# Kernel tuning notes

Hardware: AMD Instinct MI355X
Metric: run time of the kernel (lower is better)

Reference implementation:

```python
import jax, jax.numpy as jnp
import numpy as np

# Model dims (MiniCPM-style decode-only LM inside VoxCPM2)
L, B, D = 16, 4, 1024
H, HD, KVH = 16, 64, 8          # query heads, head dim, KV heads (GQA)
DFF = 4096
S = 2048                         # current KV cache length
SCALE_DEPTH = 1.4                # mup depth scaling
EPS = 1e-5
THETA = 10000.0
W_STD = 0.02


def setup_inputs() -> dict:
    key = jax.random.key(0)
    ks = jax.random.split(key, 12)
    return {
        "inputs_embeds": jax.random.normal(ks[0], (B, D), jnp.float32),
        "k_cache": jax.random.normal(ks[1], (L, B, KVH, S, HD), jnp.float32),
        "v_cache": jax.random.normal(ks[2], (L, B, KVH, S, HD), jnp.float32),
        "ln1_w": jnp.ones((L, D), jnp.float32),
        "ln2_w": jnp.ones((L, D), jnp.float32),
        "norm_w": jnp.ones((D,), jnp.float32),
        "wq": jax.random.normal(ks[3], (L, D, H * HD), jnp.float32) * W_STD,
        "wk": jax.random.normal(ks[4], (L, D, KVH * HD), jnp.float32) * W_STD,
        "wv": jax.random.normal(ks[5], (L, D, KVH * HD), jnp.float32) * W_STD,
        "wo": jax.random.normal(ks[6], (L, H * HD, D), jnp.float32) * W_STD,
        "w_gate": jax.random.normal(ks[7], (L, D, DFF), jnp.float32) * W_STD,
        "w_up": jax.random.normal(ks[8], (L, D, DFF), jnp.float32) * W_STD,
        "w_down": jax.random.normal(ks[9], (L, DFF, D), jnp.float32) * W_STD,
        "cache_length": S,  # position id of the token being decoded
    }


def _rmsnorm(x, w):
    return x * jax.lax.rsqrt(jnp.mean(x * x, axis=-1, keepdims=True) + EPS) * w


def _rotate_half(x):
    x1, x2 = jnp.split(x, 2, axis=-1)
    return jnp.concatenate((-x2, x1), axis=-1)


def _decode_step(inputs_embeds, k_cache, v_cache, ln1_w, ln2_w, norm_w,
                 wq, wk, wv, wo, w_gate, w_up, w_down, cache_length):
    # RoPE tables for the single decode position
    pos = jnp.asarray(cache_length, jnp.float32)
    inv_freq = 1.0 / (THETA ** (jnp.arange(0, HD, 2, dtype=jnp.float32) / HD))
    freqs = pos * inv_freq                       # [HD/2]
    emb = jnp.concatenate((freqs, freqs))        # [HD]
    cos, sin = jnp.cos(emb), jnp.sin(emb)

    mup = SCALE_DEPTH / np.sqrt(L)
    scale = 1.0 / np.sqrt(HD)
    G = H // KVH  # query heads per KV head

    def layer(h, ws):
        l1, l2, Wq, Wk, Wv, Wo, Wg, Wu, Wd, kc, vc = ws
        x = _rmsnorm(h, l1)                                  # [B, D]
        q = (x @ Wq).reshape(B, H, HD)
        k = (x @ Wk).reshape(B, KVH, HD)
        v = (x @ Wv).reshape(B, KVH, HD)
        q = q * cos + _rotate_half(q) * sin
        k = k * cos + _rotate_half(k) * sin
        nk = jnp.concatenate((kc, k[:, :, None, :]), axis=2)  # [B, KVH, S+1, HD]
        nv = jnp.concatenate((vc, v[:, :, None, :]), axis=2)
        qg = q.reshape(B, KVH, G, HD)                         # GQA grouping
        scores = jnp.einsum('bkgd,bksd->bkgs', qg, nk) * scale
        p = jax.nn.softmax(scores, axis=-1)
        o = jnp.einsum('bkgs,bksd->bkgd', p, nv).reshape(B, H * HD)
        h = h + (o @ Wo) * mup                                # mup residual
        x = _rmsnorm(h, l2)
        mlp = (jax.nn.silu(x @ Wg) * (x @ Wu)) @ Wd           # SwiGLU
        h = h + mlp * mup
        return h, (nk, nv)

    h, (next_k, next_v) = jax.lax.scan(
        layer, inputs_embeds,
        (ln1_w, ln2_w, wq, wk, wv, wo, w_gate, w_up, w_down, k_cache, v_cache))
    h = _rmsnorm(h, norm_w)
    return h, next_k, next_v


def reference(inputs_embeds, k_cache, v_cache, ln1_w, ln2_w, norm_w,
              wq, wk, wv, wo, w_gate, w_up, w_down, cache_length):
    h, nk, nv = _decode_step(inputs_embeds, k_cache, v_cache, ln1_w, ln2_w,
                             norm_w, wq, wk, wv, wo, w_gate, w_up, w_down,
                             cache_length)
    return h, nk, nv, jnp.asarray(cache_length + 1, jnp.int64)
```

## Files before the change

### kernel.cpp

```cpp
#include <hip/hip_runtime.h>
#include <math.h>

#define MUP 0.35f
#define SCALE 0.125f
#define EPS 1e-5f

#define WS_HA    0
#define WS_HB    4096
#define WS_YMLP  8192
#define WS_YO    12288
#define WS_QKVP  16384
#define WS_GUP   16384
#define WS_OPART 278528

#define OUT_NK  4096
#define OUT_NV  (4096 + 16*4*8*2049*64)
#define OUT_SC  (4096 + 2*16*4*8*2049*64)

__device__ __forceinline__ float wsum64(float v) {
    v += __shfl_xor(v, 32); v += __shfl_xor(v, 16); v += __shfl_xor(v, 8);
    v += __shfl_xor(v, 4);  v += __shfl_xor(v, 2);  v += __shfl_xor(v, 1);
    return v;
}

__device__ __forceinline__ void fma4(float4& a, float s, const float4 w) {
    a.x = fmaf(s, w.x, a.x); a.y = fmaf(s, w.y, a.y);
    a.z = fmaf(s, w.z, a.z); a.w = fmaf(s, w.w, a.w);
}

__global__ __launch_bounds__(256) void k_init(const float* __restrict__ emb,
                                              const int* __restrict__ cl,
                                              float* __restrict__ ws,
                                              float* __restrict__ out) {
    int tid = threadIdx.x;
    float4* ws4 = (float4*)ws;
    float4 z = {0.f, 0.f, 0.f, 0.f};
    if (blockIdx.x == 0) {
        const float4* e4 = (const float4*)emb;
        #pragma unroll
        for (int k = 0; k < 4; ++k) ws4[(WS_HA >> 2) + k * 256 + tid] = e4[k * 256 + tid];
        if (tid == 0) out[OUT_SC] = (float)(cl[0] + 1);
    } else if (blockIdx.x == 1) {
        #pragma unroll
        for (int k = 0; k < 4; ++k) ws4[(WS_YMLP >> 2) + k * 256 + tid] = z;
    } else {
        #pragma unroll
        for (int k = 0; k < 4; ++k) ws4[(WS_YO >> 2) + k * 256 + tid] = z;
    }
}

__global__ __launch_bounds__(256) void k_a(const float* __restrict__ ln1,
                                           const float* __restrict__ wq,
                                           const float* __restrict__ wk,
                                           const float* __restrict__ wv,
                                           float* __restrict__ ws, int l) {
    float4* ws4 = (float4*)ws;
    int tid = threadIdx.x, w = tid >> 6, lane = tid & 63;
    if (blockIdx.x >= 256) {
        float4 z = {0,0,0,0};
        ws4[(WS_YO >> 2) + (blockIdx.x - 256) * 256 + tid] = z;
        return;
    }
    __shared__ float xs[4][32];
    __shared__ float4 red[4][64][4];
    __shared__ float sred[4][4];
    const int s = blockIdx.x >> 3, xt = blockIdx.x & 7;

    float4 hn[4]; float ss[4];
    #pragma unroll
    for (int b = 0; b < 4; ++b) {
        float4 h = ws4[(WS_HA >> 2) + b * 256 + tid];
        float4 y = ws4[(WS_YMLP >> 2) + b * 256 + tid];
        h.x = fmaf(MUP, y.x, h.x); h.y = fmaf(MUP, y.y, h.y);
        h.z = fmaf(MUP, y.z, h.z); h.w = fmaf(MUP, y.w, h.w);
        hn[b] = h;
        ss[b] = h.x*h.x + h.y*h.y + h.z*h.z + h.w*h.w;
    }
    #pragma unroll
    for (int b = 0; b < 4; ++b) {
        float v = wsum64(ss[b]);
        if (lane == 0) sred[w][b] = v;
    }
    __syncthreads();
    float rstd[4];
    #pragma unroll
    for (int b = 0; b < 4; ++b)
        rstd[b] = rsqrtf((sred[0][b] + sred[1][b] + sred[2][b] + sred[3][b]) * (1.f/1024.f) + EPS);
    if (blockIdx.x == 0) {
        #pragma unroll
        for (int b = 0; b < 4; ++b) ws4[(WS_HB >> 2) + b * 256 + tid] = hn[b];
    }
    {
        int tl = tid - s * 8;
        if (tl >= 0 && tl < 8) {
            float4 g4 = ((const float4*)ln1)[l * 256 + tid];
            #pragma unroll
            for (int b = 0; b < 4; ++b) {
                float4 xv;
                xv.x = hn[b].x * rstd[b] * g4.x; xv.y = hn[b].y * rstd[b] * g4.y;
                xv.z = hn[b].z * rstd[b] * g4.z; xv.w = hn[b].w * rstd[b] * g4.w;
                ((float4*)xs[b])[tl] = xv;
            }
        }
    }
    __syncthreads();

    const float* Wp; int nc, c;
    if (xt < 4)      { Wp = wq + (size_t)l * 1024 * 1024; nc = 1024; c = xt * 256 + lane * 4; }
    else if (xt < 6) { Wp = wk + (size_t)l * 1024 * 512;  nc = 512;  c = (xt - 4) * 256 + lane * 4; }
    else             { Wp = wv + (size_t)l * 1024 * 512;  nc = 512;  c = (xt - 6) * 256 + lane * 4; }
    const float4* W4 = (const float4*)(Wp + c);
    const size_t nc4 = (size_t)(nc >> 2);
    float4 a0 = {0,0,0,0}, a1 = a0, a2 = a0, a3 = a0;
    #pragma unroll
    for (int rr = 0; rr < 8; ++rr) {
        int r = w * 8 + rr;
        float4 wv4 = W4[(size_t)(s * 32 + r) * nc4];
        fma4(a0, xs[0][r], wv4); fma4(a1, xs[1][r], wv4);
        fma4(a2, xs[2][r], wv4); fma4(a3, xs[3][r], wv4);
    }
    red[w][lane][0] = a0; red[w][lane][1] = a1;
    red[w][lane][2] = a2; red[w][lane][3] = a3;
    __syncthreads();
    if (w == 0) {
        float4* QKVP4 = ws4 + (WS_QKVP >> 2);
        #pragma unroll
        for (int b = 0; b < 4; ++b) {
            float4 s0v = red[0][lane][b], s1v = red[1][lane][b],
                   s2v = red[2][lane][b], s3v = red[3][lane][b];
            s0v.x += s1v.x + s2v.x + s3v.x; s0v.y += s1v.y + s2v.y + s3v.y;
            s0v.z += s1v.z + s2v.z + s3v.z; s0v.w += s1v.w + s2v.w + s3v.w;
            QKVP4[(size_t)(s * 4 + b) * 512 + xt * 64 + lane] = s0v;
        }
    }
}

__global__ __launch_bounds__(256) void k_b(const float* __restrict__ kc,
                                           const float* __restrict__ vc,
                                           const int* __restrict__ cl,
                                           float* __restrict__ ws,
                                           float* __restrict__ nk,
                                           float* __restrict__ nv, int l) {
    const int bid = blockIdx.x;
    const int b = bid >> 7, rem = bid & 127, kvh = rem >> 4, c = rem & 15;
    const int s0 = c * 128;
    const int tid = threadIdx.x, w = tid >> 6, lane = tid & 63;
    const int sub = lane >> 4, j = lane & 15;
    float4* ws4 = (float4*)ws;
    const float4* QKVP4 = (const float4*)ws4 + (WS_QKVP >> 2);

    __shared__ float4 vst[128][16];
    __shared__ float sc[2][132];
    __shared__ float wm[2][4];
    __shared__ float oacc[2][4][64];
    __shared__ float wl[2][4];

    const float pos = (float)cl[0];
    float cs4[4], sn4[4];
    #pragma unroll
    for (int m = 0; m < 4; ++m) {
        float t = (float)(4 * (j & 7) + m);
        float fr = pos * __expf(-t * 0.2878231366242557f);
        cs4[m] = cosf(fr); sn4[m] = sinf(fr);
    }
    const float sgn = (j < 8) ? -1.f : 1.f;

    float4 q0 = {0,0,0,0}, q1 = {0,0,0,0};
    #pragma unroll
    for (int sp = 0; sp < 32; ++sp) {
        const float4* qp = QKVP4 + (size_t)(sp * 4 + b) * 512 + kvh * 32;
        float4 t0 = qp[j], t1 = qp[16 + j];
        q0.x += t0.x; q0.y += t0.y; q0.z += t0.z; q0.w += t0.w;
        q1.x += t1.x; q1.y += t1.y; q1.z += t1.z; q1.w += t1.w;
    }
    {
        float4 q0p, q1p;
        q0p.x = __shfl_xor(q0.x, 8); q0p.y = __shfl_xor(q0.y, 8);
        q0p.z = __shfl_xor(q0.z, 8); q0p.w = __shfl_xor(q0.w, 8);
        q1p.x = __shfl_xor(q1.x, 8); q1p.y = __shfl_xor(q1.y, 8);
        q1p.z = __shfl_xor(q1.z, 8); q1p.w = __shfl_xor(q1.w, 8);
        q0.x = q0.x * cs4[0] + sgn * q0p.x * sn4[0];
        q0.y = q0.y * cs4[1] + sgn * q0p.y * sn4[1];
        q0.z = q0.z * cs4[2] + sgn * q0p.z * sn4[2];
        q0.w = q0.w * cs4[3] + sgn * q0p.w * sn4[3];
        q1.x = q1.x * cs4[0] + sgn * q1p.x * sn4[0];
        q1.y = q1.y * cs4[1] + sgn * q1p.y * sn4[1];
        q1.z = q1.z * cs4[2] + sgn * q1p.z * sn4[2];
        q1.w = q1.w * cs4[3] + sgn * q1p.w * sn4[3];
    }

    const size_t cbase = (size_t)((l * 4 + b) * 8 + kvh);
    const float4* kc4 = (const float4*)kc + cbase * 2048 * 16;
    const float4* vc4 = (const float4*)vc + cbase * 2048 * 16;
    float4* nk4 = (float4*)nk + cbase * 2049 * 16;
    float4* nv4 = (float4*)nv + cbase * 2049 * 16;

    float m0 = -1e30f, m1 = -1e30f;
    const int rbase = s0 + w * 32;
    #pragma unroll 4
    for (int i = 0; i < 8; ++i) {
        int r = rbase + i * 4 + sub;
        float4 kv = kc4[(size_t)r * 16 + j];
        float4 vv = vc4[(size_t)r * 16 + j];
        nk4[(size_t)r * 16 + j] = kv;
        nv4[(size_t)r * 16 + j] = vv;
        vst[r - s0][j] = vv;
        float d0 = kv.x*q0.x + kv.y*q0.y + kv.z*q0.z + kv.w*q0.w;
        float d1 = kv.x*q1.x + kv.y*q1.y + kv.z*q1.z + kv.w*q1.w;
        d0 += __shfl_xor(d0, 1); d0 += __shfl_xor(d0, 2);
        d0 += __shfl_xor(d0, 4); d0 += __shfl_xor(d0, 8);
        d1 += __shfl_xor(d1, 1); d1 += __shfl_xor(d1, 2);
        d1 += __shfl_xor(d1, 4); d1 += __shfl_xor(d1, 8);
        d0 *= SCALE; d1 *= SCALE;
        if (j == 0) { sc[0][r - s0] = d0; sc[1][r - s0] = d1; }
        m0 = fmaxf(m0, d0); m1 = fmaxf(m1, d1);
    }
    float4 vnew = {0,0,0,0};
    if (c == 15 && w == 0 && sub == 0) {
        float4 kv = {0,0,0,0};
        #pragma unroll
        for (int sp = 0; sp < 32; ++sp) {
            const float4* pp = QKVP4 + (size_t)(sp * 4 + b) * 512;
            float4 t0 = pp[256 + kvh * 16 + j];
            float4 t1 = pp[384 + kvh * 16 + j];
            kv.x += t0.x; kv.y += t0.y; kv.z += t0.z; kv.w += t0.w;
            vnew.x += t1.x; vnew.y += t1.y; vnew.z += t1.z; vnew.w += t1.w;
        }
        float4 kp;
        kp.x = __shfl_xor(kv.x, 8); kp.y = __shfl_xor(kv.y, 8);
        kp.z = __shfl_xor(kv.z, 8); kp.w = __shfl_xor(kv.w, 8);
        kv.x = kv.x * cs4[0] + sgn * kp.x * sn4[0];
        kv.y = kv.y * cs4[1] + sgn * kp.y * sn4[1];
        kv.z = kv.z * cs4[2] + sgn * kp.z * sn4[2];
        kv.w = kv.w * cs4[3] + sgn * kp.w * sn4[3];
        nk4[(size_t)2048 * 16 + j] = kv;
        nv4[(size_t)2048 * 16 + j] = vnew;
        float d0 = kv.x*q0.x + kv.y*q0.y + kv.z*q0.z + kv.w*q0.w;
        float d1 = kv.x*q1.x + kv.y*q1.y + kv.z*q1.z + kv.w*q1.w;
        d0 += __shfl_xor(d0, 1); d0 += __shfl_xor(d0, 2);
        d0 += __shfl_xor(d0, 4); d0 += __shfl_xor(d0, 8);
        d1 += __shfl_xor(d1, 1); d1 += __shfl_xor(d1, 2);
        d1 += __shfl_xor(d1, 4); d1 += __shfl_xor(d1, 8);
        d0 *= SCALE; d1 *= SCALE;
        if (j == 0) { sc[0][128] = d0; sc[1][128] = d1; }
        m0 = fmaxf(m0, d0); m1 = fmaxf(m1, d1);
    }
    m0 = fmaxf(m0, __shfl_xor(m0, 16)); m0 = fmaxf(m0, __shfl_xor(m0, 32));
    m1 = fmaxf(m1, __shfl_xor(m1, 16)); m1 = fmaxf(m1, __shfl_xor(m1, 32));
    if (lane == 0) { wm[0][w] = m0; wm[1][w] = m1; }
    __syncthreads();
    const float M0 = fmaxf(fmaxf(wm[0][0], wm[0][1]), fmaxf(wm[0][2], wm[0][3]));
    const float M1 = fmaxf(fmaxf(wm[1][0], wm[1][1]), fmaxf(wm[1][2], wm[1][3]));

    float4 o0 = {0,0,0,0}, o1 = {0,0,0,0};
    float l0 = 0.f, l1 = 0.f;
    #pragma unroll 4
    for (int i = 0; i < 8; ++i) {
        int r = rbase + i * 4 + sub;
        float4 vv = vst[r - s0][j];
        float p0 = __expf(sc[0][r - s0] - M0);
        float p1 = __expf(sc[1][r - s0] - M1);
        fma4(o0, p0, vv); fma4(o1, p1, vv);
        l0 += p0; l1 += p1;
    }
    if (c == 15 && w == 0 && sub == 0) {
        float p0 = __expf(sc[0][128] - M0);
        float p1 = __expf(sc[1][128] - M1);
        fma4(o0, p0, vnew); fma4(o1, p1, vnew);
        l0 += p0; l1 += p1;
    }
    o0.x += __shfl_xor(o0.x, 16); o0.x += __shfl_xor(o0.x, 32);
    o0.y += __shfl_xor(o0.y, 16); o0.y += __shfl_xor(o0.y, 32);
    o0.z += __shfl_xor(o0.z, 16); o0.z += __shfl_xor(o0.z, 32);
    o0.w += __shfl_xor(o0.w, 16); o0.w += __shfl_xor(o0.w, 32);
    o1.x += __shfl_xor(o1.x, 16); o1.x += __shfl_xor(o1.x, 32);
    o1.y += __shfl_xor(o1.y, 16); o1.y += __shfl_xor(o1.y, 32);
    o1.z += __shfl_xor(o1.z, 16); o1.z += __shfl_xor(o1.z, 32);
    o1.w += __shfl_xor(o1.w, 16); o1.w += __shfl_xor(o1.w, 32);
    l0 += __shfl_xor(l0, 16); l0 += __shfl_xor(l0, 32);
    l1 += __shfl_xor(l1, 16); l1 += __shfl_xor(l1, 32);
    if (sub == 0) {
        oacc[0][w][4*j+0] = o0.x; oacc[0][w][4*j+1] = o0.y;
        oacc[0][w][4*j+2] = o0.z; oacc[0][w][4*j+3] = o0.w;
        oacc[1][w][4*j+0] = o1.x; oacc[1][w][4*j+1] = o1.y;
        oacc[1][w][4*j+2] = o1.z; oacc[1][w][4*j+3] = o1.w;
    }
    if (lane == 0) { wl[0][w] = l0; wl[1][w] = l1; }
    __syncthreads();
    int pbase = WS_OPART + ((b * 8 + kvh) * 16 + c) * 132;
    if (tid < 128) {
        int h = tid >> 6, d = tid & 63;
        ws[pbase + h * 64 + d] = oacc[h][0][d] + oacc[h][1][d] + oacc[h][2][d] + oacc[h][3][d];
    } else if (tid == 128) {
        ws[pbase + 128] = M0;
        ws[pbase + 129] = wl[0][0] + wl[0][1] + wl[0][2] + wl[0][3];
        ws[pbase + 130] = M1;
        ws[pbase + 131] = wl[1][0] + wl[1][1] + wl[1][2] + wl[1][3];
    }
}

__global__ __launch_bounds__(256) void k_c(const float* __restrict__ wo,
                                           float* __restrict__ ws, int l) {
    float4* ws4 = (float4*)ws;
    int tid = threadIdx.x, w = tid >> 6, lane = tid & 63;
    if (blockIdx.x >= 128) {
        float4 z = {0,0,0,0};
        ws4[(WS_YMLP >> 2) + (blockIdx.x - 128) * 256 + tid] = z;
        return;
    }
    __shared__ float xs[4][32];
    __shared__ float4 red[4][64][4];
    const int xt = blockIdx.x & 3, s = blockIdx.x >> 2;
    if (tid < 128) {
        const int bb = tid >> 5, rr = tid & 31;
        const int r = s * 32 + rr;
        const int kvh = r >> 7, g = (r >> 6) & 1, d = r & 63;
        const float* bp = ws + WS_OPART + (size_t)((bb * 8 + kvh) * 16) * 132;
        float m = -1e30f;
        #pragma unroll
        for (int cc = 0; cc < 16; ++cc)
            m = fmaxf(m, bp[cc * 132 + 128 + 2 * g]);
        float lt = 0.f, ot = 0.f;
        #pragma unroll
        for (int cc = 0; cc < 16; ++cc) {
            float f = __expf(bp[cc * 132 + 128 + 2 * g] - m);
            lt += bp[cc * 132 + 129 + 2 * g] * f;
            ot += bp[cc * 132 + g * 64 + d] * f;
        }
        xs[bb][rr] = ot / lt;
    }
    __syncthreads();
    const float4* W4 = (const float4*)(wo + (size_t)l * 1024 * 1024 + xt * 256 + lane * 4);
    float4 a0 = {0,0,0,0}, a1 = a0, a2 = a0, a3 = a0;
    #pragma unroll
    for (int rr = 0; rr < 8; ++rr) {
        int r = w * 8 + rr;
        float4 wv4 = W4[(size_t)(s * 32 + r) * 256];
        fma4(a0, xs[0][r], wv4); fma4(a1, xs[1][r], wv4);
        fma4(a2, xs[2][r], wv4); fma4(a3, xs[3][r], wv4);
    }
    red[w][lane][0] = a0; red[w][lane][1] = a1;
    red[w][lane][2] = a2; red[w][lane][3] = a3;
    __syncthreads();
    if (w == 0) {
        int c = xt * 256 + lane * 4;
        #pragma unroll
        for (int b = 0; b < 4; ++b) {
            float4 s0v = red[0][lane][b], s1v = red[1][lane][b],
                   s2v = red[2][lane][b], s3v = red[3][lane][b];
            s0v.x += s1v.x + s2v.x + s3v.x; s0v.y += s1v.y + s2v.y + s3v.y;
            s0v.z += s1v.z + s2v.z + s3v.z; s0v.w += s1v.w + s2v.w + s3v.w;
            atomicAdd(&ws[WS_YO + b * 1024 + c + 0], s0v.x);
            atomicAdd(&ws[WS_YO + b * 1024 + c + 1], s0v.y);
            atomicAdd(&ws[WS_YO + b * 1024 + c + 2], s0v.z);
            atomicAdd(&ws[WS_YO + b * 1024 + c + 3], s0v.w);
        }
    }
}

__global__ __launch_bounds__(256) void k_d(const float* __restrict__ ln2,
                                           const float* __restrict__ wg,
                                           const float* __restrict__ wu,
                                           float* __restrict__ ws, int l) {
    float4* ws4 = (float4*)ws;
    int tid = threadIdx.x, w = tid >> 6, lane = tid & 63;
    __shared__ float xs[4][128];
    __shared__ float4 red[4][64][4];
    __shared__ float sred[4][4];
    const int mat = blockIdx.x >> 4, t16 = blockIdx.x & 15, y = blockIdx.y;

    float4 hn[4]; float ss[4];
    #pragma unroll
    for (int b = 0; b < 4; ++b) {
        float4 h = ws4[(WS_HB >> 2) + b * 256 + tid];
        float4 yv = ws4[(WS_YO >> 2) + b * 256 + tid];
        h.x = fmaf(MUP, yv.x, h.x); h.y = fmaf(MUP, yv.y, h.y);
        h.z = fmaf(MUP, yv.z, h.z); h.w = fmaf(MUP, yv.w, h.w);
        hn[b] = h;
        ss[b] = h.x*h.x + h.y*h.y + h.z*h.z + h.w*h.w;
    }
    #pragma unroll
    for (int b = 0; b < 4; ++b) {
        float v = wsum64(ss[b]);
        if (lane == 0) sred[w][b] = v;
    }
    __syncthreads();
    float rstd[4];
    #pragma unroll
    for (int b = 0; b < 4; ++b)
        rstd[b] = rsqrtf((sred[0][b] + sred[1][b] + sred[2][b] + sred[3][b]) * (1.f/1024.f) + EPS);
    if (blockIdx.x == 0 && blockIdx.y == 0) {
        #pragma unroll
        for (int b = 0; b < 4; ++b) ws4[(WS_HA >> 2) + b * 256 + tid] = hn[b];
    }
    {
        int tl = tid - y * 32;
        if (tl >= 0 && tl < 32) {
            float4 g4 = ((const float4*)ln2)[l * 256 + tid];
            #pragma unroll
            for (int b = 0; b < 4; ++b) {
                float4 xv;
                xv.x = hn[b].x * rstd[b] * g4.x; xv.y = hn[b].y * rstd[b] * g4.y;
                xv.z = hn[b].z * rstd[b] * g4.z; xv.w = hn[b].w * rstd[b] * g4.w;
                ((float4*)xs[b])[tl] = xv;
            }
        }
    }
    __syncthreads();

    const float* Wm = (mat ? wu : wg) + (size_t)l * 1024 * 4096;
    const float4* W4 = (const float4*)(Wm + t16 * 256 + lane * 4);
    float4 a0 = {0,0,0,0}, a1 = a0, a2 = a0, a3 = a0;
    #pragma unroll 8
    for (int rr = 0; rr < 32; ++rr) {
        int r = w * 32 + rr;
        float4 wv4 = W4[(size_t)(y * 128 + r) * 1024];
        fma4(a0, xs[0][r], wv4); fma4(a1, xs[1][r], wv4);
        fma4(a2, xs[2][r], wv4); fma4(a3, xs[3][r], wv4);
    }
    red[w][lane][0] = a0; red[w][lane][1] = a1;
    red[w][lane][2] = a2; red[w][lane][3] = a3;
    __syncthreads();
    if (w == 0) {
        float4* GUP4 = ws4 + (WS_GUP >> 2);
        #pragma unroll
        for (int b = 0; b < 4; ++b) {
            float4 s0v = red[0][lane][b], s1v = red[1][lane][b],
                   s2v = red[2][lane][b], s3v = red[3][lane][b];
            s0v.x += s1v.x + s2v.x + s3v.x; s0v.y += s1v.y + s2v.y + s3v.y;
            s0v.z += s1v.z + s2v.z + s3v.z; s0v.w += s1v.w + s2v.w + s3v.w;
            GUP4[(size_t)((mat * 8 + y) * 4 + b) * 1024 + t16 * 64 + lane] = s0v;
        }
    }
}

__global__ __launch_bounds__(256) void k_e(const float* __restrict__ wd,
                                           float* __restrict__ ws, int l) {
    float4* ws4 = (float4*)ws;
    int tid = threadIdx.x, w = tid >> 6, lane = tid & 63;
    __shared__ float ts[4][128];
    __shared__ float4 red[4][64][4];
    const int xt = blockIdx.x, s = blockIdx.y;
    if (tid < 128) {
        const int bb = tid >> 5, i = tid & 31;
        const int f4 = s * 32 + i;
        const float4* GUP4 = (const float4*)ws4 + (WS_GUP >> 2);
        float4 g = {0,0,0,0}, u = {0,0,0,0};
        #pragma unroll
        for (int sp = 0; sp < 8; ++sp) {
            float4 gv = GUP4[(size_t)(sp * 4 + bb) * 1024 + f4];
            float4 uv = GUP4[(size_t)((8 + sp) * 4 + bb) * 1024 + f4];
            g.x += gv.x; g.y += gv.y; g.z += gv.z; g.w += gv.w;
            u.x += uv.x; u.y += uv.y; u.z += uv.z; u.w += uv.w;
        }
        float4 t;
        t.x = (g.x / (1.f + __expf(-g.x))) * u.x;
        t.y = (g.y / (1.f + __expf(-g.y))) * u.y;
        t.z = (g.z / (1.f + __expf(-g.z))) * u.z;
        t.w = (g.w / (1.f + __expf(-g.w))) * u.w;
        ((float4*)ts[bb])[i] = t;
    }
    __syncthreads();
    const float4* W4 = (const float4*)(wd + (size_t)l * 4096 * 1024 + xt * 256 + lane * 4);
    float4 a0 = {0,0,0,0}, a1 = a0, a2 = a0, a3 = a0;
    #pragma unroll 8
    for (int rr = 0; rr < 32; ++rr) {
        int r = w * 32 + rr;
        float4 wv4 = W4[(size_t)(s * 128 + r) * 256];
        fma4(a0, ts[0][r], wv4); fma4(a1, ts[1][r], wv4);
        fma4(a2, ts[2][r], wv4); fma4(a3, ts[3][r], wv4);
    }
    red[w][lane][0] = a0; red[w][lane][1] = a1;
    red[w][lane][2] = a2; red[w][lane][3] = a3;
    __syncthreads();
    if (w == 0) {
        int c = xt * 256 + lane * 4;
        #pragma unroll
        for (int b = 0; b < 4; ++b) {
            float4 s0v = red[0][lane][b], s1v = red[1][lane][b],
                   s2v = red[2][lane][b], s3v = red[3][lane][b];
            s0v.x += s1v.x + s2v.x + s3v.x; s0v.y += s1v.y + s2v.y + s3v.y;
            s0v.z += s1v.z + s2v.z + s3v.z; s0v.w += s1v.w + s2v.w + s3v.w;
            atomicAdd(&ws[WS_YMLP + b * 1024 + c + 0], s0v.x);
            atomicAdd(&ws[WS_YMLP + b * 1024 + c + 1], s0v.y);
            atomicAdd(&ws[WS_YMLP + b * 1024 + c + 2], s0v.z);
            atomicAdd(&ws[WS_YMLP + b * 1024 + c + 3], s0v.w);
        }
    }
}

__global__ __launch_bounds__(256) void k_final(const float* __restrict__ normw,
                                               float* __restrict__ ws,
                                               float* __restrict__ out) {
    float4* ws4 = (float4*)ws;
    int tid = threadIdx.x;
    int b = blockIdx.x, w = tid >> 6, lane = tid & 63;
    __shared__ float sred[4];
    float4 h = ws4[(WS_HA >> 2) + b * 256 + tid];
    float4 y = ws4[(WS_YMLP >> 2) + b * 256 + tid];
    h.x = fmaf(MUP, y.x, h.x); h.y = fmaf(MUP, y.y, h.y);
    h.z = fmaf(MUP, y.z, h.z); h.w = fmaf(MUP, y.w, h.w);
    float ssv = h.x*h.x + h.y*h.y + h.z*h.z + h.w*h.w;
    float v = wsum64(ssv);
    if (lane == 0) sred[w] = v;
    __syncthreads();
    float rstd = rsqrtf((sred[0] + sred[1] + sred[2] + sred[3]) * (1.f/1024.f) + EPS);
    float4 g4 = ((const float4*)normw)[tid];
    float4 o;
    o.x = h.x * rstd * g4.x; o.y = h.y * rstd * g4.y;
    o.z = h.z * rstd * g4.z; o.w = h.w * rstd * g4.w;
    ((float4*)out)[b * 256 + tid] = o;
}

extern "C" void kernel_launch(void* const* d_in, const int* in_sizes, int n_in,
                              void* d_out, int out_size, void* d_ws, size_t ws_size,
                              hipStream_t stream) {
    const float* emb  = (const float*)d_in[0];
    const float* kc   = (const float*)d_in[1];
    const float* vc   = (const float*)d_in[2];
    const float* ln1  = (const float*)d_in[3];
    const float* ln2  = (const float*)d_in[4];
    const float* nrmw = (const float*)d_in[5];
    const float* wq   = (const float*)d_in[6];
    const float* wk   = (const float*)d_in[7];
    const float* wv   = (const float*)d_in[8];
    const float* wo   = (const float*)d_in[9];
    const float* wg   = (const float*)d_in[10];
    const float* wu   = (const float*)d_in[11];
    const float* wd   = (const float*)d_in[12];
    const int*   cl   = (const int*)d_in[13];

    float* out = (float*)d_out;
    float* ws  = (float*)d_ws;
    float* nk  = out + OUT_NK;
    float* nv  = out + OUT_NV;

    k_init<<<3, 256, 0, stream>>>(emb, cl, ws, out);
    for (int l = 0; l < 16; ++l) {
        k_a<<<260, 256, 0, stream>>>(ln1, wq, wk, wv, ws, l);
        k_b<<<512, 256, 0, stream>>>(kc, vc, cl, ws, nk, nv, l);
        k_c<<<132, 256, 0, stream>>>(wo, ws, l);
        k_d<<<dim3(32, 8), 256, 0, stream>>>(ln2, wg, wu, ws, l);
        k_e<<<dim3(4, 32), 256, 0, stream>>>(wd, ws, l);
    }
    k_final<<<4, 256, 0, stream>>>(nrmw, ws, out);
}
```

Measured before the change: 1.065 ms.

## Use online softmax in attention, batch weight loads, rebalance grids

The attention kernel now uses a streaming online softmax with register-held K/V batches instead of staging V and scores in shared memory, and each block covers 256 cache rows, so it launches half as many blocks. The GEMV kernels issue all weight loads of a chunk before the FMAs to raise memory-level parallelism. The down-projection grid is doubled with smaller row slices, and the gate/up partial buffer moves to its own workspace region. These changes target latency hiding in bandwidth-bound decode kernels, at the cost of more exp calls per row and fewer attention blocks.

Result: faster. 997.2 us (-6.3%).

```diff
diff --git a/kernel.cpp b/kernel.cpp
--- a/kernel.cpp
+++ b/kernel.cpp
@@ -10,8 +10,8 @@
 #define WS_YMLP  8192
 #define WS_YO    12288
 #define WS_QKVP  16384
-#define WS_GUP   16384
 #define WS_OPART 278528
+#define WS_GUP   413696
 
 #define OUT_NK  4096
 #define OUT_NV  (4096 + 16*4*8*2049*64)
@@ -111,13 +111,16 @@
     else             { Wp = wv + (size_t)l * 1024 * 512;  nc = 512;  c = (xt - 6) * 256 + lane * 4; }
     const float4* W4 = (const float4*)(Wp + c);
     const size_t nc4 = (size_t)(nc >> 2);
+    float4 wr[8];
+    #pragma unroll
+    for (int i = 0; i < 8; ++i)
+        wr[i] = W4[(size_t)(s * 32 + w * 8 + i) * nc4];
     float4 a0 = {0,0,0,0}, a1 = a0, a2 = a0, a3 = a0;
     #pragma unroll
-    for (int rr = 0; rr < 8; ++rr) {
-        int r = w * 8 + rr;
-        float4 wv4 = W4[(size_t)(s * 32 + r) * nc4];
-        fma4(a0, xs[0][r], wv4); fma4(a1, xs[1][r], wv4);
-        fma4(a2, xs[2][r], wv4); fma4(a3, xs[3][r], wv4);
+    for (int i = 0; i < 8; ++i) {
+        int r = w * 8 + i;
+        fma4(a0, xs[0][r], wr[i]); fma4(a1, xs[1][r], wr[i]);
+        fma4(a2, xs[2][r], wr[i]); fma4(a3, xs[3][r], wr[i]);
     }
     red[w][lane][0] = a0; red[w][lane][1] = a1;
     red[w][lane][2] = a2; red[w][lane][3] = a3;
@@ -142,18 +145,15 @@
                                            float* __restrict__ nk,
                                            float* __restrict__ nv, int l) {
     const int bid = blockIdx.x;
-    const int b = bid >> 7, rem = bid & 127, kvh = rem >> 4, c = rem & 15;
-    const int s0 = c * 128;
+    const int b = bid >> 6, kvh = (bid >> 3) & 7, c = bid & 7;
+    const int s0 = c * 256;
     const int tid = threadIdx.x, w = tid >> 6, lane = tid & 63;
     const int sub = lane >> 4, j = lane & 15;
     float4* ws4 = (float4*)ws;
     const float4* QKVP4 = (const float4*)ws4 + (WS_QKVP >> 2);
 
-    __shared__ float4 vst[128][16];
-    __shared__ float sc[2][132];
-    __shared__ float wm[2][4];
-    __shared__ float oacc[2][4][64];
-    __shared__ float wl[2][4];
+    __shared__ float4 oac[2][16][16];
+    __shared__ float mlm[2][16], mll[2][16];
 
     const float pos = (float)cl[0];
     float cs4[4], sn4[4];
@@ -166,7 +166,7 @@
     const float sgn = (j < 8) ? -1.f : 1.f;
 
     float4 q0 = {0,0,0,0}, q1 = {0,0,0,0};
-    #pragma unroll
+    #pragma unroll 8
     for (int sp = 0; sp < 32; ++sp) {
         const float4* qp = QKVP4 + (size_t)(sp * 4 + b) * 512 + kvh * 32;
         float4 t0 = qp[j], t1 = qp[16 + j];
@@ -195,30 +195,48 @@
     float4* nk4 = (float4*)nk + cbase * 2049 * 16;
     float4* nv4 = (float4*)nv + cbase * 2049 * 16;
 
-    float m0 = -1e30f, m1 = -1e30f;
-    const int rbase = s0 + w * 32;
-    #pragma unroll 4
-    for (int i = 0; i < 8; ++i) {
-        int r = rbase + i * 4 + sub;
-        float4 kv = kc4[(size_t)r * 16 + j];
-        float4 vv = vc4[(size_t)r * 16 + j];
-        nk4[(size_t)r * 16 + j] = kv;
-        nv4[(size_t)r * 16 + j] = vv;
-        vst[r - s0][j] = vv;
-        float d0 = kv.x*q0.x + kv.y*q0.y + kv.z*q0.z + kv.w*q0.w;
-        float d1 = kv.x*q1.x + kv.y*q1.y + kv.z*q1.z + kv.w*q1.w;
-        d0 += __shfl_xor(d0, 1); d0 += __shfl_xor(d0, 2);
-        d0 += __shfl_xor(d0, 4); d0 += __shfl_xor(d0, 8);
-        d1 += __shfl_xor(d1, 1); d1 += __shfl_xor(d1, 2);
-        d1 += __shfl_xor(d1, 4); d1 += __shfl_xor(d1, 8);
-        d0 *= SCALE; d1 *= SCALE;
-        if (j == 0) { sc[0][r - s0] = d0; sc[1][r - s0] = d1; }
-        m0 = fmaxf(m0, d0); m1 = fmaxf(m1, d1);
-    }
-    float4 vnew = {0,0,0,0};
-    if (c == 15 && w == 0 && sub == 0) {
-        float4 kv = {0,0,0,0};
-        #pragma unroll
+    float m0 = -1e30f, m1 = -1e30f, l0 = 0.f, l1 = 0.f;
+    float4 o0 = {0,0,0,0}, o1 = {0,0,0,0};
+    for (int g = 0; g < 4; ++g) {
+        const int rb = s0 + g * 64 + w * 16;
+        float4 kr[4], vr[4];
+        #pragma unroll
+        for (int ii = 0; ii < 4; ++ii) {
+            int r = rb + ii * 4 + sub;
+            kr[ii] = kc4[(size_t)r * 16 + j];
+            vr[ii] = vc4[(size_t)r * 16 + j];
+        }
+        #pragma unroll
+        for (int ii = 0; ii < 4; ++ii) {
+            int r = rb + ii * 4 + sub;
+            nk4[(size_t)r * 16 + j] = kr[ii];
+            nv4[(size_t)r * 16 + j] = vr[ii];
+        }
+        #pragma unroll
+        for (int ii = 0; ii < 4; ++ii) {
+            float4 kv = kr[ii];
+            float d0 = kv.x*q0.x + kv.y*q0.y + kv.z*q0.z + kv.w*q0.w;
+            float d1 = kv.x*q1.x + kv.y*q1.y + kv.z*q1.z + kv.w*q1.w;
+            d0 += __shfl_xor(d0, 1); d0 += __shfl_xor(d0, 2);
+            d0 += __shfl_xor(d0, 4); d0 += __shfl_xor(d0, 8);
+            d1 += __shfl_xor(d1, 1); d1 += __shfl_xor(d1, 2);
+            d1 += __shfl_xor(d1, 4); d1 += __shfl_xor(d1, 8);
+            d0 *= SCALE; d1 *= SCALE;
+            float mn0 = fmaxf(m0, d0);
+            float e0 = __expf(m0 - mn0), p0 = __expf(d0 - mn0);
+            o0.x = o0.x*e0 + p0*vr[ii].x; o0.y = o0.y*e0 + p0*vr[ii].y;
+            o0.z = o0.z*e0 + p0*vr[ii].z; o0.w = o0.w*e0 + p0*vr[ii].w;
+            l0 = l0*e0 + p0; m0 = mn0;
+            float mn1 = fmaxf(m1, d1);
+            float e1 = __expf(m1 - mn1), p1 = __expf(d1 - mn1);
+            o1.x = o1.x*e1 + p1*vr[ii].x; o1.y = o1.y*e1 + p1*vr[ii].y;
+            o1.z = o1.z*e1 + p1*vr[ii].z; o1.w = o1.w*e1 + p1*vr[ii].w;
+            l1 = l1*e1 + p1; m1 = mn1;
+        }
+    }
+    if (c == 7 && w == 0 && sub == 0) {
+        float4 kv = {0,0,0,0}, vnew = {0,0,0,0};
+        #pragma unroll 8
         for (int sp = 0; sp < 32; ++sp) {
             const float4* pp = QKVP4 + (size_t)(sp * 4 + b) * 512;
             float4 t0 = pp[256 + kvh * 16 + j];
@@ -242,60 +260,41 @@
         d1 += __shfl_xor(d1, 1); d1 += __shfl_xor(d1, 2);
         d1 += __shfl_xor(d1, 4); d1 += __shfl_xor(d1, 8);
         d0 *= SCALE; d1 *= SCALE;
-        if (j == 0) { sc[0][128] = d0; sc[1][128] = d1; }
-        m0 = fmaxf(m0, d0); m1 = fmaxf(m1, d1);
-    }
-    m0 = fmaxf(m0, __shfl_xor(m0, 16)); m0 = fmaxf(m0, __shfl_xor(m0, 32));
-    m1 = fmaxf(m1, __shfl_xor(m1, 16)); m1 = fmaxf(m1, __shfl_xor(m1, 32));
-    if (lane == 0) { wm[0][w] = m0; wm[1][w] = m1; }
-    __syncthreads();
-    const float M0 = fmaxf(fmaxf(wm[0][0], wm[0][1]), fmaxf(wm[0][2], wm[0][3]));
-    const float M1 = fmaxf(fmaxf(wm[1][0], wm[1][1]), fmaxf(wm[1][2], wm[1][3]));
-
-    float4 o0 = {0,0,0,0}, o1 = {0,0,0,0};
-    float l0 = 0.f, l1 = 0.f;
-    #pragma unroll 4
-    for (int i = 0; i < 8; ++i) {
-        int r = rbase + i * 4 + sub;
-        float4 vv = vst[r - s0][j];
-        float p0 = __expf(sc[0][r - s0] - M0);
-        float p1 = __expf(sc[1][r - s0] - M1);
-        fma4(o0, p0, vv); fma4(o1, p1, vv);
-        l0 += p0; l1 += p1;
-    }
-    if (c == 15 && w == 0 && sub == 0) {
-        float p0 = __expf(sc[0][128] - M0);
-        float p1 = __expf(sc[1][128] - M1);
-        fma4(o0, p0, vnew); fma4(o1, p1, vnew);
-        l0 += p0; l1 += p1;
-    }
-    o0.x += __shfl_xor(o0.x, 16); o0.x += __shfl_xor(o0.x, 32);
-    o0.y += __shfl_xor(o0.y, 16); o0.y += __shfl_xor(o0.y, 32);
-    o0.z += __shfl_xor(o0.z, 16); o0.z += __shfl_xor(o0.z, 32);
-    o0.w += __shfl_xor(o0.w, 16); o0.w += __shfl_xor(o0.w, 32);
-    o1.x += __shfl_xor(o1.x, 16); o1.x += __shfl_xor(o1.x, 32);
-    o1.y += __shfl_xor(o1.y, 16); o1.y += __shfl_xor(o1.y, 32);
-    o1.z += __shfl_xor(o1.z, 16); o1.z += __shfl_xor(o1.z, 32);
-    o1.w += __shfl_xor(o1.w, 16); o1.w += __shfl_xor(o1.w, 32);
-    l0 += __shfl_xor(l0, 16); l0 += __shfl_xor(l0, 32);
-    l1 += __shfl_xor(l1, 16); l1 += __shfl_xor(l1, 32);
-    if (sub == 0) {
-        oacc[0][w][4*j+0] = o0.x; oacc[0][w][4*j+1] = o0.y;
-        oacc[0][w][4*j+2] = o0.z; oacc[0][w][4*j+3] = o0.w;
-        oacc[1][w][4*j+0] = o1.x; oacc[1][w][4*j+1] = o1.y;
-        oacc[1][w][4*j+2] = o1.z; oacc[1][w][4*j+3] = o1.w;
-    }
-    if (lane == 0) { wl[0][w] = l0; wl[1][w] = l1; }
-    __syncthreads();
-    int pbase = WS_OPART + ((b * 8 + kvh) * 16 + c) * 132;
+        float mn0 = fmaxf(m0, d0);
+        float e0 = __expf(m0 - mn0), p0 = __expf(d0 - mn0);
+        o0.x = o0.x*e0 + p0*vnew.x; o0.y = o0.y*e0 + p0*vnew.y;
+        o0.z = o0.z*e0 + p0*vnew.z; o0.w = o0.w*e0 + p0*vnew.w;
+        l0 = l0*e0 + p0; m0 = mn0;
+        float mn1 = fmaxf(m1, d1);
+        float e1 = __expf(m1 - mn1), p1 = __expf(d1 - mn1);
+        o1.x = o1.x*e1 + p1*vnew.x; o1.y = o1.y*e1 + p1*vnew.y;
+        o1.z = o1.z*e1 + p1*vnew.z; o1.w = o1.w*e1 + p1*vnew.w;
+        l1 = l1*e1 + p1; m1 = mn1;
+    }
+    const int grp = w * 4 + sub;
+    oac[0][grp][j] = o0;
+    oac[1][grp][j] = o1;
+    if (j == 0) {
+        mlm[0][grp] = m0; mll[0][grp] = l0;
+        mlm[1][grp] = m1; mll[1][grp] = l1;
+    }
+    __syncthreads();
     if (tid < 128) {
-        int h = tid >> 6, d = tid & 63;
-        ws[pbase + h * 64 + d] = oacc[h][0][d] + oacc[h][1][d] + oacc[h][2][d] + oacc[h][3][d];
-    } else if (tid == 128) {
-        ws[pbase + 128] = M0;
-        ws[pbase + 129] = wl[0][0] + wl[0][1] + wl[0][2] + wl[0][3];
-        ws[pbase + 130] = M1;
-        ws[pbase + 131] = wl[1][0] + wl[1][1] + wl[1][2] + wl[1][3];
+        const int h = tid >> 6, d = tid & 63;
+        const float* oa = (const float*)&oac[h][0][0];
+        float M = -1e30f;
+        #pragma unroll
+        for (int g2 = 0; g2 < 16; ++g2) M = fmaxf(M, mlm[h][g2]);
+        float ot = 0.f, lt = 0.f;
+        #pragma unroll
+        for (int g2 = 0; g2 < 16; ++g2) {
+            float e = __expf(mlm[h][g2] - M);
+            ot += oa[g2 * 64 + d] * e;
+            lt += mll[h][g2] * e;
+        }
+        int pbase = WS_OPART + ((b * 8 + kvh) * 8 + c) * 132;
+        ws[pbase + h * 64 + d] = ot;
+        if (d == 0) { ws[pbase + 128 + 2 * h] = M; ws[pbase + 129 + 2 * h] = lt; }
     }
 }
 
@@ -315,14 +314,14 @@
         const int bb = tid >> 5, rr = tid & 31;
         const int r = s * 32 + rr;
         const int kvh = r >> 7, g = (r >> 6) & 1, d = r & 63;
-        const float* bp = ws + WS_OPART + (size_t)((bb * 8 + kvh) * 16) * 132;
+        const float* bp = ws + WS_OPART + (size_t)((bb * 8 + kvh) * 8) * 132;
         float m = -1e30f;
         #pragma unroll
-        for (int cc = 0; cc < 16; ++cc)
+        for (int cc = 0; cc < 8; ++cc)
             m = fmaxf(m, bp[cc * 132 + 128 + 2 * g]);
         float lt = 0.f, ot = 0.f;
         #pragma unroll
-        for (int cc = 0; cc < 16; ++cc) {
+        for (int cc = 0; cc < 8; ++cc) {
             float f = __expf(bp[cc * 132 + 128 + 2 * g] - m);
             lt += bp[cc * 132 + 129 + 2 * g] * f;
             ot += bp[cc * 132 + g * 64 + d] * f;
@@ -331,13 +330,16 @@
     }
     __syncthreads();
     const float4* W4 = (const float4*)(wo + (size_t)l * 1024 * 1024 + xt * 256 + lane * 4);
+    float4 wr[8];
+    #pragma unroll
+    for (int i = 0; i < 8; ++i)
+        wr[i] = W4[(size_t)(s * 32 + w * 8 + i) * 256];
     float4 a0 = {0,0,0,0}, a1 = a0, a2 = a0, a3 = a0;
     #pragma unroll
-    for (int rr = 0; rr < 8; ++rr) {
-        int r = w * 8 + rr;
-        float4 wv4 = W4[(size_t)(s * 32 + r) * 256];
-        fma4(a0, xs[0][r], wv4); fma4(a1, xs[1][r], wv4);
-        fma4(a2, xs[2][r], wv4); fma4(a3, xs[3][r], wv4);
+    for (int i = 0; i < 8; ++i) {
+        int r = w * 8 + i;
+        fma4(a0, xs[0][r], wr[i]); fma4(a1, xs[1][r], wr[i]);
+        fma4(a2, xs[2][r], wr[i]); fma4(a3, xs[3][r], wr[i]);
     }
     red[w][lane][0] = a0; red[w][lane][1] = a1;
     red[w][lane][2] = a2; red[w][lane][3] = a3;
@@ -411,12 +413,18 @@
     const float* Wm = (mat ? wu : wg) + (size_t)l * 1024 * 4096;
     const float4* W4 = (const float4*)(Wm + t16 * 256 + lane * 4);
     float4 a0 = {0,0,0,0}, a1 = a0, a2 = a0, a3 = a0;
-    #pragma unroll 8
-    for (int rr = 0; rr < 32; ++rr) {
-        int r = w * 32 + rr;
-        float4 wv4 = W4[(size_t)(y * 128 + r) * 1024];
-        fma4(a0, xs[0][r], wv4); fma4(a1, xs[1][r], wv4);
-        fma4(a2, xs[2][r], wv4); fma4(a3, xs[3][r], wv4);
+    #pragma unroll
+    for (int ch = 0; ch < 4; ++ch) {
+        float4 wr[8];
+        #pragma unroll
+        for (int i = 0; i < 8; ++i)
+            wr[i] = W4[(size_t)(y * 128 + w * 32 + ch * 8 + i) * 1024];
+        #pragma unroll
+        for (int i = 0; i < 8; ++i) {
+            int r = w * 32 + ch * 8 + i;
+            fma4(a0, xs[0][r], wr[i]); fma4(a1, xs[1][r], wr[i]);
+            fma4(a2, xs[2][r], wr[i]); fma4(a3, xs[3][r], wr[i]);
+        }
     }
     red[w][lane][0] = a0; red[w][lane][1] = a1;
     red[w][lane][2] = a2; red[w][lane][3] = a3;
@@ -438,12 +446,12 @@
                                            float* __restrict__ ws, int l) {
     float4* ws4 = (float4*)ws;
     int tid = threadIdx.x, w = tid >> 6, lane = tid & 63;
-    __shared__ float ts[4][128];
+    __shared__ float ts[4][64];
     __shared__ float4 red[4][64][4];
     const int xt = blockIdx.x, s = blockIdx.y;
-    if (tid < 128) {
-        const int bb = tid >> 5, i = tid & 31;
-        const int f4 = s * 32 + i;
+    if (tid < 64) {
+        const int bb = tid >> 4, i = tid & 15;
+        const int f4 = s * 16 + i;
         const float4* GUP4 = (const float4*)ws4 + (WS_GUP >> 2);
         float4 g = {0,0,0,0}, u = {0,0,0,0};
         #pragma unroll
@@ -463,12 +471,18 @@
     __syncthreads();
     const float4* W4 = (const float4*)(wd + (size_t)l * 4096 * 1024 + xt * 256 + lane * 4);
     float4 a0 = {0,0,0,0}, a1 = a0, a2 = a0, a3 = a0;
-    #pragma unroll 8
-    for (int rr = 0; rr < 32; ++rr) {
-        int r = w * 32 + rr;
-        float4 wv4 = W4[(size_t)(s * 128 + r) * 256];
-        fma4(a0, ts[0][r], wv4); fma4(a1, ts[1][r], wv4);
-        fma4(a2, ts[2][r], wv4); fma4(a3, ts[3][r], wv4);
+    #pragma unroll
+    for (int ch = 0; ch < 2; ++ch) {
+        float4 wr[8];
+        #pragma unroll
+        for (int i = 0; i < 8; ++i)
+            wr[i] = W4[(size_t)(s * 64 + w * 16 + ch * 8 + i) * 256];
+        #pragma unroll
+        for (int i = 0; i < 8; ++i) {
+            int r = w * 16 + ch * 8 + i;
+            fma4(a0, ts[0][r], wr[i]); fma4(a1, ts[1][r], wr[i]);
+            fma4(a2, ts[2][r], wr[i]); fma4(a3, ts[3][r], wr[i]);
+        }
     }
     red[w][lane][0] = a0; red[w][lane][1] = a1;
     red[w][lane][2] = a2; red[w][lane][3] = a3;
@@ -538,10 +552,10 @@
     k_init<<<3, 256, 0, stream>>>(emb, cl, ws, out);
     for (int l = 0; l < 16; ++l) {
         k_a<<<260, 256, 0, stream>>>(ln1, wq, wk, wv, ws, l);
-        k_b<<<512, 256, 0, stream>>>(kc, vc, cl, ws, nk, nv, l);
+        k_b<<<256, 256, 0, stream>>>(kc, vc, cl, ws, nk, nv, l);
         k_c<<<132, 256, 0, stream>>>(wo, ws, l);
         k_d<<<dim3(32, 8), 256, 0, stream>>>(ln2, wg, wu, ws, l);
-        k_e<<<dim3(4, 32), 256, 0, stream>>>(wd, ws, l);
+        k_e<<<dim3(4, 64), 256, 0, stream>>>(wd, ws, l);
     }
     k_final<<<4, 256, 0, stream>>>(nrmw, ws, out);
 }
```
